# Kernel tuning notes

Hardware: AMD Instinct MI355X
Metric: run time of the kernel (lower is better)

The kernel has to match this reference:

```python
import jax, jax.numpy as jnp
import numpy as np

H = 8          # head_count
C = 512        # emb_dim
DH = C // H    # head_emb_size = 64
FF = 4 * C     # feed_forward hidden = 2048
EPS = 1e-5     # nn.LayerNorm default eps


def setup_inputs() -> dict:
    key = jax.random.key(0)
    ks = jax.random.split(key, 16)
    s = lambda fan_in: 1.0 / np.sqrt(fan_in)
    inp = {
        "x": jax.random.normal(ks[0], (4, 2048, C), dtype=jnp.float32),
        "ln1_g": jnp.ones((C,), jnp.float32),
        "ln1_b": jnp.zeros((C,), jnp.float32),
        # per-head QKV projections, stacked over heads: [H, C, DH]
        "Wq": jax.random.uniform(ks[1], (H, C, DH), jnp.float32, -s(C), s(C)),
        "bq": jax.random.uniform(ks[2], (H, DH), jnp.float32, -s(C), s(C)),
        "Wk": jax.random.uniform(ks[3], (H, C, DH), jnp.float32, -s(C), s(C)),
        "bk": jax.random.uniform(ks[4], (H, DH), jnp.float32, -s(C), s(C)),
        "Wv": jax.random.uniform(ks[5], (H, C, DH), jnp.float32, -s(C), s(C)),
        "bv": jax.random.uniform(ks[6], (H, DH), jnp.float32, -s(C), s(C)),
        "Wp": jax.random.uniform(ks[7], (C, C), jnp.float32, -s(C), s(C)),
        "bp": jax.random.uniform(ks[8], (C,), jnp.float32, -s(C), s(C)),
        "ln2_g": jnp.ones((C,), jnp.float32),
        "ln2_b": jnp.zeros((C,), jnp.float32),
        "W1": jax.random.uniform(ks[9], (C, FF), jnp.float32, -s(C), s(C)),
        "b1": jax.random.uniform(ks[10], (FF,), jnp.float32, -s(C), s(C)),
        "W2": jax.random.uniform(ks[11], (FF, C), jnp.float32, -s(FF), s(FF)),
        "b2": jax.random.uniform(ks[12], (C,), jnp.float32, -s(FF), s(FF)),
    }
    return inp


def _layernorm(x, g, b):
    mu = jnp.mean(x, axis=-1, keepdims=True)
    var = jnp.mean((x - mu) ** 2, axis=-1, keepdims=True)
    return (x - mu) * jax.lax.rsqrt(var + EPS) * g + b


def _block(x, ln1_g, ln1_b, Wq, bq, Wk, bk, Wv, bv, Wp, bp, ln2_g, ln2_b, W1, b1, W2, b2):
    B, T, _ = x.shape
    h = _layernorm(x, ln1_g, ln1_b)
    # per-head projections, vectorized over heads: [B,H,T,DH]
    Q = jnp.einsum("btc,hcd->bhtd", h, Wq) + bq[None, :, None, :]
    K = jnp.einsum("btc,hcd->bhtd", h, Wk) + bk[None, :, None, :]
    V = jnp.einsum("btc,hcd->bhtd", h, Wv) + bv[None, :, None, :]
    wei = jnp.einsum("bhtd,bhsd->bhts", Q, K) / jnp.sqrt(jnp.float32(DH))
    causal = jnp.tril(jnp.ones((T, T), dtype=bool))
    wei = jnp.where(causal, wei, jnp.float32(-1e9))  # masked_fill(-1e9)
    wei = jax.nn.softmax(wei, axis=-1)
    out = jnp.einsum("bhts,bhsd->bhtd", wei, V)      # [B,H,T,DH]
    # concat heads (head order = ModuleList order) -> [B,T,C]
    out = out.transpose(0, 2, 1, 3).reshape(B, T, H * DH)
    attn = out @ Wp + bp
    x = x + attn
    h2 = _layernorm(x, ln2_g, ln2_b)
    ff = jax.nn.relu(h2 @ W1 + b1) @ W2 + b2
    return x + ff


def reference(x, ln1_g, ln1_b, Wq, bq, Wk, bk, Wv, bv, Wp, bp, ln2_g, ln2_b, W1, b1, W2, b2):
    return _block(x, ln1_g, ln1_b, Wq, bq, Wk, bk, Wv, bv, Wp, bp, ln2_g, ln2_b, W1, b1, W2, b2)
```

## Files before the change

### kernel.cpp

```cpp
#include <hip/hip_runtime.h>

typedef unsigned short u16;
typedef unsigned int   u32;
typedef __attribute__((ext_vector_type(4))) int   i32x4;
typedef __attribute__((ext_vector_type(4))) float f32x4;
typedef __attribute__((ext_vector_type(4))) unsigned short u16x4;
typedef __attribute__((ext_vector_type(8))) unsigned short u16x8;

#define DEVI static __device__ __forceinline__

DEVI u16 f2b(float f) {
  u32 u = __builtin_bit_cast(u32, f);
  return (u16)((u + 0x7FFFu + ((u >> 16) & 1u)) >> 16);
}

DEVI void mfma16(f32x4& d, i32x4 a, i32x4 b) {
  asm("v_mfma_f32_16x16x32_bf16 %0, %1, %2, %0" : "+v"(d) : "v"(a), "v"(b));
}

DEVI void gload16(const void* g, void* l) {
  __builtin_amdgcn_global_load_lds(
      (const __attribute__((address_space(1))) void*)g,
      (__attribute__((address_space(3))) void*)l, 16, 0, 0);
}

DEVI int swz(int row, int b) {
  return (row << 7) + (((b >> 4) ^ (row & 7)) << 4) + (b & 15);
}

__global__ __launch_bounds__(256) void trans_tile(
    const float* __restrict__ src, u16* __restrict__ dst, int R, int C)
{
  __shared__ u16 tile[64][72];
  const int rb = blockIdx.x * 64, cb = blockIdx.y * 64;
  const int t = threadIdx.x;
  const int tr = t >> 2, tc = (t & 3) * 16;
  const float* sp = src + (size_t)(rb + tr) * C + cb + tc;
  #pragma unroll
  for (int q = 0; q < 4; q++) {
    float4 v = *(const float4*)(sp + q * 4);
    tile[tr][tc + q*4 + 0] = f2b(v.x);
    tile[tr][tc + q*4 + 1] = f2b(v.y);
    tile[tr][tc + q*4 + 2] = f2b(v.z);
    tile[tr][tc + q*4 + 3] = f2b(v.w);
  }
  __syncthreads();
  const int dc = t >> 2, dr = (t & 3) * 16;
  u16x8 o0, o1;
  #pragma unroll
  for (int j = 0; j < 8; j++) { o0[j] = tile[dr + j][dc]; o1[j] = tile[dr + 8 + j][dc]; }
  u16* dp = dst + (size_t)(cb + dc) * R + rb + dr;
  *(u16x8*)(dp) = o0;
  *(u16x8*)(dp + 8) = o1;
}

__global__ __launch_bounds__(256) void pack_qkv_tile(
    const float* __restrict__ Wq, const float* __restrict__ Wk,
    const float* __restrict__ Wv, u16* __restrict__ dst)
{
  __shared__ u16 tile[64][72];
  const int bid = blockIdx.x;
  const int cb = (bid & 7) * 64, h = (bid >> 3) & 7, widx = bid >> 6;
  const float* W = (widx == 0) ? Wq : (widx == 1) ? Wk : Wv;
  const float* src = W + (size_t)h * 512 * 64;
  const int t = threadIdx.x;
  const int tr = t >> 2, tc = (t & 3) * 16;
  const float* sp = src + (size_t)(cb + tr) * 64 + tc;
  #pragma unroll
  for (int q = 0; q < 4; q++) {
    float4 v = *(const float4*)(sp + q * 4);
    tile[tr][tc + q*4 + 0] = f2b(v.x);
    tile[tr][tc + q*4 + 1] = f2b(v.y);
    tile[tr][tc + q*4 + 2] = f2b(v.z);
    tile[tr][tc + q*4 + 3] = f2b(v.w);
  }
  __syncthreads();
  const int dc = t >> 2, dr = (t & 3) * 16;
  u16x8 o0, o1;
  #pragma unroll
  for (int j = 0; j < 8; j++) { o0[j] = tile[dr + j][dc]; o1[j] = tile[dr + 8 + j][dc]; }
  u16* dp = dst + (size_t)(widx * 512 + h * 64 + dc) * 512 + cb + dr;
  *(u16x8*)(dp) = o0;
  *(u16x8*)(dp + 8) = o1;
}

__global__ __launch_bounds__(256) void ln_kernel(
    const float* __restrict__ x, const float* __restrict__ gamma,
    const float* __restrict__ beta, u16* __restrict__ out)
{
  const int lane = threadIdx.x & 63;
  const int row = blockIdx.x * 4 + (threadIdx.x >> 6);
  const float4* xr = (const float4*)(x + (size_t)row * 512) + lane * 2;
  float4 a0 = xr[0], a1 = xr[1];
  float s  = a0.x + a0.y + a0.z + a0.w + a1.x + a1.y + a1.z + a1.w;
  float sq = a0.x*a0.x + a0.y*a0.y + a0.z*a0.z + a0.w*a0.w
           + a1.x*a1.x + a1.y*a1.y + a1.z*a1.z + a1.w*a1.w;
  #pragma unroll
  for (int o = 32; o > 0; o >>= 1) { s += __shfl_xor(s, o); sq += __shfl_xor(sq, o); }
  const float mu = s * (1.0f / 512.0f);
  const float rstd = rsqrtf(sq * (1.0f / 512.0f) - mu * mu + 1e-5f);
  const float4* g4 = (const float4*)gamma + lane * 2;
  const float4* b4 = (const float4*)beta  + lane * 2;
  float4 g0 = g4[0], g1 = g4[1], b0 = b4[0], b1 = b4[1];
  float xv[8] = {a0.x,a0.y,a0.z,a0.w,a1.x,a1.y,a1.z,a1.w};
  float gv[8] = {g0.x,g0.y,g0.z,g0.w,g1.x,g1.y,g1.z,g1.w};
  float bv[8] = {b0.x,b0.y,b0.z,b0.w,b1.x,b1.y,b1.z,b1.w};
  u16x8 ov;
  #pragma unroll
  for (int j = 0; j < 8; j++) ov[j] = f2b((xv[j] - mu) * rstd * gv[j] + bv[j]);
  *(u16x8*)(out + (size_t)row * 512 + lane * 8) = ov;
}

template<int KD, int EPI>
__global__ __launch_bounds__(256) void gemm_bt(
    const u16* __restrict__ A, const u16* __restrict__ Bt,
    const float* __restrict__ bias0, const float* __restrict__ bias1,
    const float* __restrict__ bias2, const float* __restrict__ resid,
    void* __restrict__ out0, void* __restrict__ out1, void* __restrict__ out2)
{
  __shared__ __align__(16) u16 sA[3][128 * 32];
  __shared__ __align__(16) u16 sB[3][128 * 32];
  constexpr int NSTEP = KD / 32;
  const int tid = threadIdx.x, lane = tid & 63, w = tid >> 6;
  const int m0 = blockIdx.x * 128, n0 = blockIdx.y * 128;
  const int wr = w >> 1, wc = w & 1, r = lane & 15, gq = lane >> 4;

  f32x4 acc[4][4] = {};

  const int o0 = w * 2048 + lane * 16;
  const int row0 = o0 >> 6, kb0 = o0 & 63;
  const int o1 = o0 + 1024;
  const int row1 = o1 >> 6, kb1 = o1 & 63;
  const char* Ab = (const char*)A;
  const char* Bb = (const char*)Bt;

#define STAGE(step, buf) do {                                                \
    const int kbyte_ = (step) * 64;                                          \
    char* sAd_ = (char*)sA + (buf) * 8192 + w * 2048;                        \
    char* sBd_ = (char*)sB + (buf) * 8192 + w * 2048;                        \
    gload16(Ab + (size_t)(m0 + row0) * (KD * 2) + kbyte_ + kb0, sAd_);       \
    gload16(Ab + (size_t)(m0 + row1) * (KD * 2) + kbyte_ + kb1, sAd_ + 1024);\
    gload16(Bb + (size_t)(n0 + row0) * (KD * 2) + kbyte_ + kb0, sBd_);       \
    gload16(Bb + (size_t)(n0 + row1) * (KD * 2) + kbyte_ + kb1, sBd_ + 1024);\
  } while (0)

  STAGE(0, 0);
  STAGE(1, 1);

  for (int t = 0; t < NSTEP; t++) {
    __builtin_amdgcn_sched_barrier(0);
    __builtin_amdgcn_s_barrier();
    if (t + 2 < NSTEP) {
      STAGE(t + 2, (t + 2) % 3);
      asm volatile("s_waitcnt vmcnt(8)" ::: "memory");
    } else if (t + 1 < NSTEP) {
      asm volatile("s_waitcnt vmcnt(4)" ::: "memory");
    } else {
      asm volatile("s_waitcnt vmcnt(0)" ::: "memory");
    }
    __builtin_amdgcn_sched_barrier(0);
    __builtin_amdgcn_s_barrier();
    const u16* sAc = sA[t % 3];
    const u16* sBc = sB[t % 3];
    i32x4 af[4], bfr[4];
    #pragma unroll
    for (int i = 0; i < 4; i++)
      af[i] = *(const i32x4*)(sAc + (wr * 64 + i * 16 + r) * 32 + gq * 8);
    #pragma unroll
    for (int j = 0; j < 4; j++)
      bfr[j] = *(const i32x4*)(sBc + (wc * 64 + j * 16 + r) * 32 + gq * 8);
    #pragma unroll
    for (int i = 0; i < 4; i++)
      #pragma unroll
      for (int j = 0; j < 4; j++)
        mfma16(acc[i][j], af[i], bfr[j]);
  }
#undef STAGE

  #pragma unroll
  for (int i = 0; i < 4; i++) {
    #pragma unroll
    for (int j = 0; j < 4; j++) {
      const int mb = m0 + wr * 64 + i * 16 + gq * 4;
      const int nc = n0 + wc * 64 + j * 16 + r;
      #pragma unroll
      for (int e = 0; e < 4; e++) {
        const int m = mb + e;
        float v = acc[i][j][e];
        if (EPI == 0) {
          float bias; u16* dst;
          if (nc < 512)       { bias = bias0[nc];        dst = (u16*)out0; }
          else if (nc < 1024) { bias = bias1[nc - 512];  dst = (u16*)out1; }
          else                { bias = bias2[nc - 1024]; dst = (u16*)out2; }
          v += bias;
          const int nn = nc & 511, h = nn >> 6, d = nn & 63;
          const int bb = m >> 11, tt = m & 2047;
          dst[(size_t)((bb * 8 + h) * 2048 + tt) * 64 + d] = f2b(v);
        } else if (EPI == 1) {
          v += bias0[nc] + resid[(size_t)m * 512 + nc];
          ((float*)out0)[(size_t)m * 512 + nc] = v;
        } else {
          v += bias0[nc];
          v = fmaxf(v, 0.0f);
          ((u16*)out0)[(size_t)m * 2048 + nc] = f2b(v);
        }
      }
    }
  }
}

__global__ __launch_bounds__(256) void attn_kernel(
    const u16* __restrict__ Q, const u16* __restrict__ K,
    const u16* __restrict__ V, u16* __restrict__ O)
{
  __shared__ __align__(16) char lds[40960];
  const int tid = threadIdx.x, lane = tid & 63, w = tid >> 6;
  const int p = blockIdx.x & 15, bh = blockIdx.x >> 4;
  const int r = lane & 15, gq = lane >> 4;
  const u16* Qb = Q + (size_t)bh * (2048 * 64);
  const u16* Kb = K + (size_t)bh * (2048 * 64);
  const u16* Vb = V + (size_t)bh * (2048 * 64);
  const int bb = bh >> 3, hh = bh & 7;
  char* Pb = lds + 32768 + w * 2048;

  const int sv = (tid & 15) * 4;
  const int dv = (tid >> 4) * 4;
  u16x4 vr[4];

#define STAGEK(s0g, buf) do {                                              \
    _Pragma("unroll")                                                      \
    for (int i_ = 0; i_ < 2; i_++) {                                       \
      int o_ = w * 2048 + i_ * 1024 + lane * 16;                           \
      int so_ = o_ ^ (((o_ >> 7) & 7) << 4);                               \
      gload16((const char*)(Kb + (size_t)(s0g) * 64) + so_,                \
              lds + (buf) * 8192 + w * 2048 + i_ * 1024);                  \
    } } while (0)

#define LOADV(s0g) do {                                                    \
    _Pragma("unroll")                                                      \
    for (int j_ = 0; j_ < 4; j_++)                                         \
      vr[j_] = *(const u16x4*)(Vb + (size_t)((s0g) + sv + j_) * 64 + dv);  \
    } while (0)

#define WRITEV(buf) do {                                                   \
    _Pragma("unroll")                                                      \
    for (int dd_ = 0; dd_ < 4; dd_++) {                                    \
      u16x4 val_ = {vr[0][dd_], vr[1][dd_], vr[2][dd_], vr[3][dd_]};       \
      *(u16x4*)(lds + 16384 + (buf) * 8192 + swz(dv + dd_, sv * 2)) = val_;\
    } } while (0)

  #pragma unroll 1
  for (int half = 0; half < 2; half++) {
    const int qt = half ? p : (31 - p);
    const int q0 = qt << 6;
    const int qg = q0 + w * 16 + r;

    i32x4 qf[2];
    qf[0] = *(const i32x4*)(Qb + (size_t)(q0 + w * 16 + r) * 64 + gq * 8);
    qf[1] = *(const i32x4*)(Qb + (size_t)(q0 + w * 16 + r) * 64 + 32 + gq * 8);

    STAGEK(0, 0);
    LOADV(0);
    WRITEV(0);
    __syncthreads();

    f32x4 accO[4] = {};
    float m_run = -1e30f, l_run = 0.0f;

    for (int t = 0; t <= qt; t++) {
      const int cb = t & 1, nb = cb ^ 1;
      const bool diag = (t == qt);
      const int s0 = t << 6;
      if (!diag) {
        STAGEK(s0 + 64, nb);
        LOADV(s0 + 64);
      }

      f32x4 st[4] = {};
      const int sbmax = diag ? (w + 1) : 4;
      #pragma unroll
      for (int kd = 0; kd < 2; kd++)
        #pragma unroll
        for (int sb = 0; sb < 4; sb++)
          if (sb < sbmax) {
            i32x4 kf = *(const i32x4*)(lds + cb * 8192 + swz(sb * 16 + r, kd * 64 + gq * 16));
            mfma16(st[sb], kf, qf[kd]);
          }

      float tmax = -1e30f;
      if (diag) {
        #pragma unroll
        for (int sb = 0; sb < 4; sb++)
          #pragma unroll
          for (int e = 0; e < 4; e++) {
            int sg = s0 + sb * 16 + gq * 4 + e;
            float v = st[sb][e] * 0.125f;
            v = (sg <= qg) ? v : -1e30f;
            st[sb][e] = v;
            tmax = fmaxf(tmax, v);
          }
      } else {
        #pragma unroll
        for (int sb = 0; sb < 4; sb++)
          #pragma unroll
          for (int e = 0; e < 4; e++) {
            float v = st[sb][e] * 0.125f;
            st[sb][e] = v;
            tmax = fmaxf(tmax, v);
          }
      }
      tmax = fmaxf(tmax, __shfl_xor(tmax, 16));
      tmax = fmaxf(tmax, __shfl_xor(tmax, 32));

      if (!__all(tmax <= m_run)) {
        const float mnew = fmaxf(m_run, tmax);
        const float alpha = __expf(m_run - mnew);
        l_run *= alpha;
        float ae[4];
        #pragma unroll
        for (int e = 0; e < 4; e++) ae[e] = __shfl(alpha, gq * 4 + e);
        #pragma unroll
        for (int db = 0; db < 4; db++)
          #pragma unroll
          for (int e = 0; e < 4; e++) accO[db][e] *= ae[e];
        m_run = mnew;
      }
      float rsum = 0.0f;
      #pragma unroll
      for (int sb = 0; sb < 4; sb++)
        #pragma unroll
        for (int e = 0; e < 4; e++) {
          float pv = __expf(st[sb][e] - m_run);
          st[sb][e] = pv;
          rsum += pv;
        }
      rsum += __shfl_xor(rsum, 16);
      rsum += __shfl_xor(rsum, 32);
      l_run += rsum;

      #pragma unroll
      for (int sb = 0; sb < 4; sb++) {
        u32 lo, hi;
        asm("v_cvt_pk_bf16_f32 %0, %1, %2" : "=v"(lo) : "v"(st[sb][0]), "v"(st[sb][1]));
        asm("v_cvt_pk_bf16_f32 %0, %1, %2" : "=v"(hi) : "v"(st[sb][2]), "v"(st[sb][3]));
        uint2 pk; pk.x = lo; pk.y = hi;
        *(uint2*)(Pb + swz(r, sb * 32 + gq * 8)) = pk;
      }

      const int kmax = diag ? ((w >> 1) + 1) : 2;
      #pragma unroll
      for (int ks = 0; ks < 2; ks++)
        if (ks < kmax) {
          i32x4 pf = *(const i32x4*)(Pb + swz(r, ks * 64 + gq * 16));
          #pragma unroll
          for (int db = 0; db < 4; db++) {
            i32x4 vf = *(const i32x4*)(lds + 16384 + cb * 8192 + swz(db * 16 + r, ks * 64 + gq * 16));
            mfma16(accO[db], pf, vf);
          }
        }

      if (!diag) WRITEV(nb);
      __syncthreads();
    }

    float le[4];
    #pragma unroll
    for (int e = 0; e < 4; e++) le[e] = 1.0f / __shfl(l_run, gq * 4 + e);
    #pragma unroll
    for (int db = 0; db < 4; db++)
      #pragma unroll
      for (int e = 0; e < 4; e++) {
        int qrow = q0 + w * 16 + gq * 4 + e;
        int d = db * 16 + r;
        O[(size_t)(bb * 2048 + qrow) * 512 + hh * 64 + d] = f2b(accO[db][e] * le[e]);
      }
  }
#undef STAGEK
#undef LOADV
#undef WRITEV
}

extern "C" void kernel_launch(void* const* d_in, const int* in_sizes, int n_in,
                              void* d_out, int out_size, void* d_ws, size_t ws_size,
                              hipStream_t stream)
{
  const float* x    = (const float*)d_in[0];
  const float* ln1g = (const float*)d_in[1];
  const float* ln1b = (const float*)d_in[2];
  const float* Wq   = (const float*)d_in[3];
  const float* bq   = (const float*)d_in[4];
  const float* Wk   = (const float*)d_in[5];
  const float* bk   = (const float*)d_in[6];
  const float* Wv   = (const float*)d_in[7];
  const float* bv   = (const float*)d_in[8];
  const float* Wp   = (const float*)d_in[9];
  const float* bp   = (const float*)d_in[10];
  const float* ln2g = (const float*)d_in[11];
  const float* ln2b = (const float*)d_in[12];
  const float* W1   = (const float*)d_in[13];
  const float* b1   = (const float*)d_in[14];
  const float* W2   = (const float*)d_in[15];
  const float* b2   = (const float*)d_in[16];

  char* ws = (char*)d_ws;
  const size_t MB = 1ull << 20;
  float* x1  = (float*)(ws);
  u16* hbuf  = (u16*)(ws + 16 * MB);
  u16* Qb    = (u16*)(ws + 24 * MB);
  u16* Kb    = (u16*)(ws + 32 * MB);
  u16* Vb    = (u16*)(ws + 40 * MB);
  u16* attn  = (u16*)(ws + 48 * MB);
  u16* fbuf  = (u16*)(ws + 24 * MB);
  u16* Wqkv  = (u16*)(ws + 56 * MB);
  u16* Wpt   = (u16*)(ws + 58 * MB);
  u16* W1t   = (u16*)(ws + 59 * MB);
  u16* W2t   = (u16*)(ws + 61 * MB);
  float* outf = (float*)d_out;

  pack_qkv_tile<<<192, 256, 0, stream>>>(Wq, Wk, Wv, Wqkv);
  trans_tile<<<dim3(8, 8),  256, 0, stream>>>(Wp, Wpt, 512, 512);
  trans_tile<<<dim3(8, 32), 256, 0, stream>>>(W1, W1t, 512, 2048);
  trans_tile<<<dim3(32, 8), 256, 0, stream>>>(W2, W2t, 2048, 512);
  ln_kernel<<<2048, 256, 0, stream>>>(x, ln1g, ln1b, hbuf);
  gemm_bt<512, 0><<<dim3(64, 12), 256, 0, stream>>>(hbuf, Wqkv, bq, bk, bv,
                                                    nullptr, Qb, Kb, Vb);
  attn_kernel<<<512, 256, 0, stream>>>(Qb, Kb, Vb, attn);
  gemm_bt<512, 1><<<dim3(64, 4), 256, 0, stream>>>(attn, Wpt, bp, nullptr, nullptr,
                                                   x, x1, nullptr, nullptr);
  ln_kernel<<<2048, 256, 0, stream>>>(x1, ln2g, ln2b, hbuf);
  gemm_bt<512, 2><<<dim3(64, 16), 256, 0, stream>>>(hbuf, W1t, b1, nullptr, nullptr,
                                                    nullptr, fbuf, nullptr, nullptr);
  gemm_bt<2048, 1><<<dim3(64, 4), 256, 0, stream>>>(fbuf, W2t, b2, nullptr, nullptr,
                                                    x1, outf, nullptr, nullptr);
}
```

Before: 177.6 us.

## Triple-buffer K/V in attention, use hardware exp2, add MFMA priority hints

The attention kernel moves from double to triple buffering of K and V tiles in LDS, prefetching two tiles ahead with explicit vmcnt waits and a single barrier per iteration. Two V register sets alternate between iterations. Softmax now folds log2(e) into the scale and calls v_exp_f32 directly instead of __expf. s_setprio hints are placed around the MFMA sections in both the GEMM and attention kernels. LDS use per block rises, which may lower occupancy.

After: 197.5 us. 1.11x slower.

```diff
diff --git a/kernel.cpp b/kernel.cpp
--- a/kernel.cpp
+++ b/kernel.cpp
@@ -12,6 +12,12 @@
 DEVI u16 f2b(float f) {
   u32 u = __builtin_bit_cast(u32, f);
   return (u16)((u + 0x7FFFu + ((u >> 16) & 1u)) >> 16);
+}
+
+DEVI float exp2_hw(float x) {
+  float r;
+  asm("v_exp_f32 %0, %1" : "=v"(r) : "v"(x));
+  return r;
 }
 
 DEVI void mfma16(f32x4& d, i32x4 a, i32x4 b) {
@@ -169,11 +175,13 @@
     #pragma unroll
     for (int j = 0; j < 4; j++)
       bfr[j] = *(const i32x4*)(sBc + (wc * 64 + j * 16 + r) * 32 + gq * 8);
+    __builtin_amdgcn_s_setprio(1);
     #pragma unroll
     for (int i = 0; i < 4; i++)
       #pragma unroll
       for (int j = 0; j < 4; j++)
         mfma16(acc[i][j], af[i], bfr[j]);
+    __builtin_amdgcn_s_setprio(0);
   }
 #undef STAGE
 
@@ -213,7 +221,7 @@
     const u16* __restrict__ Q, const u16* __restrict__ K,
     const u16* __restrict__ V, u16* __restrict__ O)
 {
-  __shared__ __align__(16) char lds[40960];
+  __shared__ __align__(16) char lds[57344];
   const int tid = threadIdx.x, lane = tid & 63, w = tid >> 6;
   const int p = blockIdx.x & 15, bh = blockIdx.x >> 4;
   const int r = lane & 15, gq = lane >> 4;
@@ -221,11 +229,12 @@
   const u16* Kb = K + (size_t)bh * (2048 * 64);
   const u16* Vb = V + (size_t)bh * (2048 * 64);
   const int bb = bh >> 3, hh = bh & 7;
-  char* Pb = lds + 32768 + w * 2048;
+  char* Pb = lds + 49152 + w * 2048;
 
   const int sv = (tid & 15) * 4;
   const int dv = (tid >> 4) * 4;
-  u16x4 vr[4];
+  u16x4 vrA[4], vrB[4];
+  const float SC2 = 0.125f * 1.44269504f;
 
 #define STAGEK(s0g, buf) do {                                              \
     _Pragma("unroll")                                                      \
@@ -236,17 +245,17 @@
               lds + (buf) * 8192 + w * 2048 + i_ * 1024);                  \
     } } while (0)
 
-#define LOADV(s0g) do {                                                    \
+#define LOADV(s0g, vr) do {                                                \
     _Pragma("unroll")                                                      \
     for (int j_ = 0; j_ < 4; j_++)                                         \
       vr[j_] = *(const u16x4*)(Vb + (size_t)((s0g) + sv + j_) * 64 + dv);  \
     } while (0)
 
-#define WRITEV(buf) do {                                                   \
+#define WRITEV(buf, vr) do {                                               \
     _Pragma("unroll")                                                      \
     for (int dd_ = 0; dd_ < 4; dd_++) {                                    \
       u16x4 val_ = {vr[0][dd_], vr[1][dd_], vr[2][dd_], vr[3][dd_]};       \
-      *(u16x4*)(lds + 16384 + (buf) * 8192 + swz(dv + dd_, sv * 2)) = val_;\
+      *(u16x4*)(lds + 24576 + (buf) * 8192 + swz(dv + dd_, sv * 2)) = val_;\
     } } while (0)
 
   #pragma unroll 1
@@ -259,33 +268,55 @@
     qf[0] = *(const i32x4*)(Qb + (size_t)(q0 + w * 16 + r) * 64 + gq * 8);
     qf[1] = *(const i32x4*)(Qb + (size_t)(q0 + w * 16 + r) * 64 + 32 + gq * 8);
 
+    __syncthreads();
+
     STAGEK(0, 0);
-    LOADV(0);
-    WRITEV(0);
-    __syncthreads();
+    LOADV(0, vrA);
+    if (qt >= 1) {
+      STAGEK(64, 1);
+      LOADV(64, vrB);
+      asm volatile("s_waitcnt vmcnt(6)" ::: "memory");
+    } else {
+      asm volatile("s_waitcnt vmcnt(0)" ::: "memory");
+    }
+    __builtin_amdgcn_sched_barrier(0);
+    WRITEV(0, vrA);
 
     f32x4 accO[4] = {};
     float m_run = -1e30f, l_run = 0.0f;
 
     for (int t = 0; t <= qt; t++) {
-      const int cb = t & 1, nb = cb ^ 1;
+      const int cbuf = t % 3;
       const bool diag = (t == qt);
       const int s0 = t << 6;
-      if (!diag) {
-        STAGEK(s0 + 64, nb);
-        LOADV(s0 + 64);
-      }
+
+      asm volatile("s_waitcnt lgkmcnt(0)" ::: "memory");
+      __builtin_amdgcn_sched_barrier(0);
+      __builtin_amdgcn_s_barrier();
+      __builtin_amdgcn_sched_barrier(0);
+
+      if (t + 2 <= qt) {
+        const int nbuf = (t + 2) % 3;
+        STAGEK(s0 + 128, nbuf);
+        if (t & 1) { LOADV(s0 + 128, vrB); } else { LOADV(s0 + 128, vrA); }
+        asm volatile("s_waitcnt vmcnt(6)" ::: "memory");
+      } else {
+        asm volatile("s_waitcnt vmcnt(0)" ::: "memory");
+      }
+      __builtin_amdgcn_sched_barrier(0);
 
       f32x4 st[4] = {};
       const int sbmax = diag ? (w + 1) : 4;
+      __builtin_amdgcn_s_setprio(1);
       #pragma unroll
       for (int kd = 0; kd < 2; kd++)
         #pragma unroll
         for (int sb = 0; sb < 4; sb++)
           if (sb < sbmax) {
-            i32x4 kf = *(const i32x4*)(lds + cb * 8192 + swz(sb * 16 + r, kd * 64 + gq * 16));
+            i32x4 kf = *(const i32x4*)(lds + cbuf * 8192 + swz(sb * 16 + r, kd * 64 + gq * 16));
             mfma16(st[sb], kf, qf[kd]);
           }
+      __builtin_amdgcn_s_setprio(0);
 
       float tmax = -1e30f;
       if (diag) {
@@ -294,7 +325,7 @@
           #pragma unroll
           for (int e = 0; e < 4; e++) {
             int sg = s0 + sb * 16 + gq * 4 + e;
-            float v = st[sb][e] * 0.125f;
+            float v = st[sb][e] * SC2;
             v = (sg <= qg) ? v : -1e30f;
             st[sb][e] = v;
             tmax = fmaxf(tmax, v);
@@ -304,7 +335,7 @@
         for (int sb = 0; sb < 4; sb++)
           #pragma unroll
           for (int e = 0; e < 4; e++) {
-            float v = st[sb][e] * 0.125f;
+            float v = st[sb][e] * SC2;
             st[sb][e] = v;
             tmax = fmaxf(tmax, v);
           }
@@ -314,7 +345,7 @@
 
       if (!__all(tmax <= m_run)) {
         const float mnew = fmaxf(m_run, tmax);
-        const float alpha = __expf(m_run - mnew);
+        const float alpha = exp2_hw(m_run - mnew);
         l_run *= alpha;
         float ae[4];
         #pragma unroll
@@ -330,7 +361,7 @@
       for (int sb = 0; sb < 4; sb++)
         #pragma unroll
         for (int e = 0; e < 4; e++) {
-          float pv = __expf(st[sb][e] - m_run);
+          float pv = exp2_hw(st[sb][e] - m_run);
           st[sb][e] = pv;
           rsum += pv;
         }
@@ -348,19 +379,23 @@
       }
 
       const int kmax = diag ? ((w >> 1) + 1) : 2;
+      __builtin_amdgcn_s_setprio(1);
       #pragma unroll
       for (int ks = 0; ks < 2; ks++)
         if (ks < kmax) {
           i32x4 pf = *(const i32x4*)(Pb + swz(r, ks * 64 + gq * 16));
           #pragma unroll
           for (int db = 0; db < 4; db++) {
-            i32x4 vf = *(const i32x4*)(lds + 16384 + cb * 8192 + swz(db * 16 + r, ks * 64 + gq * 16));
+            i32x4 vf = *(const i32x4*)(lds + 24576 + cbuf * 8192 + swz(db * 16 + r, ks * 64 + gq * 16));
             mfma16(accO[db], pf, vf);
           }
         }
-
-      if (!diag) WRITEV(nb);
-      __syncthreads();
+      __builtin_amdgcn_s_setprio(0);
+
+      if (t + 1 <= qt) {
+        const int wbuf = (t + 1) % 3;
+        if (t & 1) { WRITEV(wbuf, vrA); } else { WRITEV(wbuf, vrB); }
+      }
     }
 
     float le[4];
```
